# Optimization experiments

Measured on AMD Instinct MI355X. Metric: run time of the kernel, lower is better.

Reference implementation:

```python
import jax, jax.numpy as jnp
import numpy as np

L, B, T, D, H, FF = 4, 8, 1024, 256, 8, 1024
DK = D // H
SCALE = 1.0 / np.sqrt(DK)


def _ln(x, g, b, eps=1e-6):
    m = jnp.mean(x, axis=-1, keepdims=True)
    v = jnp.mean(jnp.square(x - m), axis=-1, keepdims=True)
    return (x - m) * jax.lax.rsqrt(v + eps) * g + b


def _l2norm(x, eps=1e-8):
    n = jnp.sqrt(jnp.sum(jnp.square(x), axis=-1, keepdims=True))
    return x / jnp.maximum(n, eps)


def setup_inputs() -> dict:
    key = jax.random.key(0)
    ks = jax.random.split(key, 8)
    s = 0.02
    inp = {
        'x': jax.random.normal(ks[0], (B, T, D), dtype=jnp.float32),
        'padding_mask': jnp.zeros((B, T), dtype=bool),
        'ln1_g': jnp.ones((L, D), jnp.float32), 'ln1_b': jnp.zeros((L, D), jnp.float32),
        'qn_g': jnp.ones((L, D), jnp.float32), 'qn_b': jnp.zeros((L, D), jnp.float32),
        'Wqkv': jax.random.normal(ks[1], (L, 3 * D, D), jnp.float32) * s,
        'bqkv': jnp.zeros((L, 3 * D), jnp.float32),
        'Wo': jax.random.normal(ks[2], (L, D, D), jnp.float32) * s,
        'bo': jnp.zeros((L, D), jnp.float32),
        'ln2_g': jnp.ones((L, D), jnp.float32), 'ln2_b': jnp.zeros((L, D), jnp.float32),
        'W1': jax.random.normal(ks[3], (L, FF, D), jnp.float32) * s,
        'b1': jnp.zeros((L, FF), jnp.float32),
        'W2': jax.random.normal(ks[4], (L, D, FF), jnp.float32) * s,
        'b2': jnp.zeros((L, D), jnp.float32),
        'alpha': jnp.full((L,), 0.1, jnp.float32),
        'beta': jnp.full((L,), 0.1, jnp.float32),
    }
    return inp


def _block(x, pad_mask, p):
    (g1, bb1, qg, qb, wqkv, bqkv, wo, bo, g2, bb2, w1, b1, w2, b2, a, be) = p
    Bn, Tn, Dn = x.shape
    # --- SemiCausalAttention on norm1(x) ---
    xn = _ln(x, g1, bb1)
    h = _ln(xn, qg, qb)                      # q_norm LayerNorm
    qkv = h @ wqkv.T + bqkv                  # [B,T,3D]
    qkv = qkv.reshape(Bn, Tn, 3, H, DK).transpose(2, 0, 3, 1, 4)  # [3,B,H,T,dk]
    Q, K, V = qkv[0], qkv[1], qkv[2]
    Q = _l2norm(Q)
    K = _l2norm(K)
    scores = jnp.einsum('bhtd,bhsd->bhts', Q, K) * SCALE
    scores = jnp.clip(scores, -10.0, 10.0)
    causal = jnp.triu(jnp.ones((Tn, Tn), dtype=bool), k=1)        # True = future
    scores = jnp.where(causal[None, None], -10000.0, scores)
    scores = jnp.where(pad_mask[:, None, None, :], -10000.0, scores)
    attn = jax.nn.softmax(scores, axis=-1)
    ao = jnp.einsum('bhts,bhsd->bhtd', attn, V)                   # [B,H,T,dk]
    ao = ao.transpose(0, 2, 1, 3).reshape(Bn, Tn, Dn)
    attn_out = (ao @ wo.T + bo) * 0.5
    x = x + jnp.tanh(a) * attn_out
    # --- FFN ---
    f = _ln(x, g2, bb2)
    f = jax.nn.gelu(f @ w1.T + b1, approximate=False)
    f = f @ w2.T + b2
    x = x + jnp.tanh(be) * f
    return jnp.clip(x, -100.0, 100.0)


def reference(x, padding_mask, ln1_g, ln1_b, qn_g, qn_b, Wqkv, bqkv, Wo, bo,
              ln2_g, ln2_b, W1, b1, W2, b2, alpha, beta):
    params = (ln1_g, ln1_b, qn_g, qn_b, Wqkv, bqkv, Wo, bo,
              ln2_g, ln2_b, W1, b1, W2, b2, alpha, beta)

    def step(carry, p):
        return _block(carry, padding_mask, p), None

    out, _ = jax.lax.scan(step, x, params)
    return out
```

## Files before the change

kernel.cpp:

```cpp
#include <hip/hip_runtime.h>
#include <hip/hip_bf16.h>
#include <math.h>

#define BB 8
#define TT 1024
#define DD 256
#define HH 8
#define BT 8192

typedef __attribute__((ext_vector_type(4))) float f32x4;
typedef __attribute__((ext_vector_type(16))) float f32x16;
typedef __attribute__((ext_vector_type(8))) short short8;
typedef __attribute__((ext_vector_type(4))) short short4v;
typedef __attribute__((ext_vector_type(8))) __bf16 bf16x8;

__device__ inline float bf2f(short s) {
  unsigned int u = ((unsigned int)(unsigned short)s) << 16;
  return __builtin_bit_cast(float, u);
}
__device__ inline short f2bf(float f) {
  unsigned int u = __builtin_bit_cast(unsigned int, f);
  unsigned int lsb = (u >> 16) & 1u;
  u += 0x7fffu + lsb;
  return (short)(u >> 16);
}
__device__ inline unsigned int cvtpk(float lo, float hi) {
  unsigned int r;
  asm("v_cvt_pk_bf16_f32 %0, %1, %2" : "=v"(r) : "v"(lo), "v"(hi));
  return r;
}

__device__ inline f32x4 mfma16(short8 a, short8 b, f32x4 c) {
  return __builtin_amdgcn_mfma_f32_16x16x32_bf16(
      __builtin_bit_cast(bf16x8, a), __builtin_bit_cast(bf16x8, b), c, 0, 0, 0);
}
__device__ inline f32x16 mfma32(short8 a, short8 b, f32x16 c) {
  return __builtin_amdgcn_mfma_f32_32x32x16_bf16(
      __builtin_bit_cast(bf16x8, a), __builtin_bit_cast(bf16x8, b), c, 0, 0, 0);
}

__device__ inline void gload_lds16(void* lds, const void* g) {
  __builtin_amdgcn_global_load_lds(
      (const __attribute__((address_space(1))) unsigned int*)g,
      (__attribute__((address_space(3))) unsigned int*)lds, 16, 0, 0);
}

__global__ __launch_bounds__(256) void cvt_all(
    const float4* __restrict__ s0, short4v* __restrict__ d0, int n0,
    const float4* __restrict__ s1, short4v* __restrict__ d1, int n1,
    const float4* __restrict__ s2, short4v* __restrict__ d2, int n2,
    const float4* __restrict__ s3, short4v* __restrict__ d3, int n3)
{
  int i = blockIdx.x * 256 + threadIdx.x;
  const float4* s; short4v* d;
  if (i < n0) { s = s0 + i; d = d0 + i; }
  else if ((i -= n0) < n1) { s = s1 + i; d = d1 + i; }
  else if ((i -= n1) < n2) { s = s2 + i; d = d2 + i; }
  else if ((i -= n2) < n3) { s = s3 + i; d = d3 + i; }
  else return;
  float4 v = *s;
  short4v o;
  o[0] = f2bf(v.x); o[1] = f2bf(v.y); o[2] = f2bf(v.z); o[3] = f2bf(v.w);
  *d = o;
}

__global__ __launch_bounds__(256) void ln_kernel(
    const float* __restrict__ Xin,
    const float* __restrict__ g1, const float* __restrict__ b1,
    const float* __restrict__ g2, const float* __restrict__ b2,
    short* __restrict__ out, int dbl)
{
  const int row = blockIdx.x * 4 + (threadIdx.x >> 6);
  const int lane = threadIdx.x & 63;
  const float4 v = *(const float4*)(Xin + (size_t)row * 256 + lane * 4);
  float y[4] = {v.x, v.y, v.z, v.w};

  float s = y[0] + y[1] + y[2] + y[3];
  #pragma unroll
  for (int m = 32; m >= 1; m >>= 1) s += __shfl_xor(s, m, 64);
  float mean = s * (1.0f / 256.0f);
  float sq = 0.f;
  #pragma unroll
  for (int i = 0; i < 4; ++i) { y[i] -= mean; sq += y[i] * y[i]; }
  #pragma unroll
  for (int m = 32; m >= 1; m >>= 1) sq += __shfl_xor(sq, m, 64);
  float rs = rsqrtf(sq * (1.0f / 256.0f) + 1e-6f);
  #pragma unroll
  for (int i = 0; i < 4; ++i) y[i] = y[i] * rs * g1[lane * 4 + i] + b1[lane * 4 + i];

  if (dbl) {
    float s2 = y[0] + y[1] + y[2] + y[3];
    #pragma unroll
    for (int m = 32; m >= 1; m >>= 1) s2 += __shfl_xor(s2, m, 64);
    float m2 = s2 * (1.0f / 256.0f);
    float sq2 = 0.f;
    #pragma unroll
    for (int i = 0; i < 4; ++i) { y[i] -= m2; sq2 += y[i] * y[i]; }
    #pragma unroll
    for (int m = 32; m >= 1; m >>= 1) sq2 += __shfl_xor(sq2, m, 64);
    float rs2 = rsqrtf(sq2 * (1.0f / 256.0f) + 1e-6f);
    #pragma unroll
    for (int i = 0; i < 4; ++i) y[i] = y[i] * rs2 * g2[lane * 4 + i] + b2[lane * 4 + i];
  }
  #pragma unroll
  for (int i = 0; i < 4; ++i) out[(size_t)row * 256 + lane * 4 + i] = f2bf(y[i]);
}

template<int BN, int EPI>
__global__ __launch_bounds__(256) void gemm_bt(
    const short* __restrict__ A, const short* __restrict__ Bw,
    const float* __restrict__ bias, float* __restrict__ X,
    short* __restrict__ Obf, const float* __restrict__ scale_p,
    int M, int N, int K)
{
  constexpr int MI = (BN == 128) ? 4 : 2;
  __shared__ __align__(16) short A_s[128 * 64];
  __shared__ __align__(16) short B_s[BN * 64];
  const int tid = threadIdx.x;
  const int lane = tid & 63;
  const int w = tid >> 6;
  const int lo4 = lane & 15, hi2 = lane >> 4;
  int wm, wn0;
  if (BN == 128) { wm = (w >> 1) * 64; wn0 = (w & 1) * 64; }
  else           { wm = w * 32;        wn0 = 0; }
  const int bid = blockIdx.x + blockIdx.y * gridDim.x;
  const int nwg = gridDim.x * gridDim.y;
  const int wg = (bid & 7) * (nwg >> 3) + (bid >> 3);
  const int tM = (wg / gridDim.x) * 128, tN = (wg % gridDim.x) * BN;

  f32x4 acc[MI][4];
  #pragma unroll
  for (int i = 0; i < MI; ++i)
    #pragma unroll
    for (int j = 0; j < 4; ++j) acc[i][j] = (f32x4){0.f, 0.f, 0.f, 0.f};

  const int swz = (lo4 & 7) << 3;

  for (int k0 = 0; k0 < K; k0 += 64) {
    #pragma unroll
    for (int ri = 0; ri < 4; ++ri) {
      int o = ri * 2048 + tid * 8;
      int row = o >> 6;
      int col = (o & 63) ^ ((row & 7) << 3);
      gload_lds16(&A_s[ri * 2048 + w * 512], A + (size_t)(tM + row) * K + k0 + col);
    }
    #pragma unroll
    for (int ri = 0; ri < BN / 32; ++ri) {
      int o = ri * 2048 + tid * 8;
      int row = o >> 6;
      int col = (o & 63) ^ ((row & 7) << 3);
      gload_lds16(&B_s[ri * 2048 + w * 512], Bw + (size_t)(tN + row) * K + k0 + col);
    }
    __syncthreads();
    #pragma unroll
    for (int kc = 0; kc < 2; ++kc) {
      short8 af[MI], bfr[4];
      #pragma unroll
      for (int i = 0; i < MI; ++i)
        af[i] = *(const short8*)&A_s[(wm + i * 16 + lo4) * 64 + ((kc * 32 + hi2 * 8) ^ swz)];
      #pragma unroll
      for (int j = 0; j < 4; ++j)
        bfr[j] = *(const short8*)&B_s[(wn0 + j * 16 + lo4) * 64 + ((kc * 32 + hi2 * 8) ^ swz)];
      #pragma unroll
      for (int i = 0; i < MI; ++i)
        #pragma unroll
        for (int j = 0; j < 4; ++j)
          acc[i][j] = mfma16(af[i], bfr[j], acc[i][j]);
    }
    __syncthreads();
  }

  if (EPI == 4) {
    #pragma unroll
    for (int i = 0; i < MI; ++i)
      #pragma unroll
      for (int j = 0; j < 4; ++j)
        #pragma unroll
        for (int r = 0; r < 4; ++r)
          acc[i][j][r] += bias[tN + wn0 + j * 16 + lo4];
    if (tN < 512) {
      const float C2 = 0.25503489702966368f;
      const float sc = (tN < 256) ? C2 : 1.0f;
      #pragma unroll
      for (int i = 0; i < MI; ++i) {
        #pragma unroll
        for (int r = 0; r < 4; ++r) {
          float s01 = acc[i][0][r] * acc[i][0][r] + acc[i][1][r] * acc[i][1][r];
          float s23 = acc[i][2][r] * acc[i][2][r] + acc[i][3][r] * acc[i][3][r];
          #pragma unroll
          for (int m = 1; m <= 8; m <<= 1) {
            s01 += __shfl_xor(s01, m, 64);
            s23 += __shfl_xor(s23, m, 64);
          }
          float n01 = sc / fmaxf(sqrtf(s01), 1e-8f);
          float n23 = sc / fmaxf(sqrtf(s23), 1e-8f);
          acc[i][0][r] *= n01; acc[i][1][r] *= n01;
          acc[i][2][r] *= n23; acc[i][3][r] *= n23;
        }
      }
    }
    #pragma unroll
    for (int i = 0; i < MI; ++i)
      #pragma unroll
      for (int j = 0; j < 4; ++j)
        #pragma unroll
        for (int r = 0; r < 4; ++r) {
          int row = tM + wm + i * 16 + hi2 * 4 + r;
          int col = tN + wn0 + j * 16 + lo4;
          Obf[(size_t)row * N + col] = f2bf(acc[i][j][r]);
        }
    return;
  }

  #pragma unroll
  for (int i = 0; i < MI; ++i) {
    #pragma unroll
    for (int j = 0; j < 4; ++j) {
      #pragma unroll
      for (int r = 0; r < 4; ++r) {
        int row = tM + wm + i * 16 + hi2 * 4 + r;
        int col = tN + wn0 + j * 16 + lo4;
        float v = acc[i][j][r] + bias[col];
        size_t idx = (size_t)row * N + col;
        if (EPI == 2) {
          float gl = 0.5f * v * (1.0f + erff(v * 0.70710678118f));
          Obf[idx] = f2bf(gl);
        } else {
          Obf[idx] = f2bf(v);
        }
      }
    }
  }
}

template<int EPI>
__global__ __launch_bounds__(256) void gemm64(
    const short* __restrict__ A, const short* __restrict__ Bw,
    const float* __restrict__ bias, float* __restrict__ X,
    const float* __restrict__ scale_p, int M, int N, int K)
{
  __shared__ __align__(16) short A_s[64 * 64];
  __shared__ __align__(16) short B_s[64 * 64];
  const int tid = threadIdx.x;
  const int lane = tid & 63;
  const int w = tid >> 6;
  const int lo4 = lane & 15, hi2 = lane >> 4;
  const int wm = (w >> 1) * 32, wn0 = (w & 1) * 32;
  const int bid = blockIdx.x + blockIdx.y * gridDim.x;
  const int nwg = gridDim.x * gridDim.y;
  const int wg = (bid & 7) * (nwg >> 3) + (bid >> 3);
  const int tM = (wg / gridDim.x) * 64, tN = (wg % gridDim.x) * 64;

  f32x4 acc[2][2];
  #pragma unroll
  for (int i = 0; i < 2; ++i)
    #pragma unroll
    for (int j = 0; j < 2; ++j) acc[i][j] = (f32x4){0.f, 0.f, 0.f, 0.f};

  const int swz = (lo4 & 7) << 3;

  for (int k0 = 0; k0 < K; k0 += 64) {
    #pragma unroll
    for (int ri = 0; ri < 2; ++ri) {
      int o = ri * 2048 + tid * 8;
      int row = o >> 6;
      int col = (o & 63) ^ ((row & 7) << 3);
      gload_lds16(&A_s[ri * 2048 + w * 512], A + (size_t)(tM + row) * K + k0 + col);
      gload_lds16(&B_s[ri * 2048 + w * 512], Bw + (size_t)(tN + row) * K + k0 + col);
    }
    __syncthreads();
    #pragma unroll
    for (int kc = 0; kc < 2; ++kc) {
      short8 af[2], bfr[2];
      #pragma unroll
      for (int i = 0; i < 2; ++i)
        af[i] = *(const short8*)&A_s[(wm + i * 16 + lo4) * 64 + ((kc * 32 + hi2 * 8) ^ swz)];
      #pragma unroll
      for (int j = 0; j < 2; ++j)
        bfr[j] = *(const short8*)&B_s[(wn0 + j * 16 + lo4) * 64 + ((kc * 32 + hi2 * 8) ^ swz)];
      #pragma unroll
      for (int i = 0; i < 2; ++i)
        #pragma unroll
        for (int j = 0; j < 2; ++j)
          acc[i][j] = mfma16(af[i], bfr[j], acc[i][j]);
    }
    __syncthreads();
  }

  float ts = tanhf(scale_p[0]);

  #pragma unroll
  for (int i = 0; i < 2; ++i) {
    #pragma unroll
    for (int j = 0; j < 2; ++j) {
      #pragma unroll
      for (int r = 0; r < 4; ++r) {
        int row = tM + wm + i * 16 + hi2 * 4 + r;
        int col = tN + wn0 + j * 16 + lo4;
        float v = acc[i][j][r] + bias[col];
        size_t idx = (size_t)row * N + col;
        if (EPI == 1) {
          X[idx] += ts * (v * 0.5f);
        } else {
          float o = X[idx] + ts * v;
          o = fminf(100.f, fmaxf(-100.f, o));
          X[idx] = o;
        }
      }
    }
  }
}

#define KG_BODY_G(KG, PKO, MASKED)                                                 \
  {                                                                                \
    const short* kp = Kbase + (size_t)(t * 64 + (KG) * 32 + lo5) * 768;            \
    short8 kf0 = *(const short8*)(kp + hi1 * 8);                                   \
    short8 kf1 = *(const short8*)(kp + 16 + hi1 * 8);                              \
    f32x16 z = (f32x16)0.0f;                                                       \
    z = mfma32(kf0, qb[0], z);                                                     \
    z = mfma32(kf1, qb[1], z);                                                     \
    float pr[16];                                                                  \
    _Pragma("unroll")                                                              \
    for (int r = 0; r < 16; ++r) {                                                 \
      float sv = __builtin_amdgcn_fmed3f(z[r], -14.4269504f, 14.4269504f);         \
      float pe;                                                                    \
      asm("v_exp_f32 %0, %1" : "=v"(pe) : "v"(sv));                                \
      const int keyrel = (r & 3) + 8 * (r >> 2) + 4 * hi1;                         \
      if (MASKED) pe = (keyrel > lo5) ? 0.f : pe;                                  \
      if (pm) pe = ((pm >> ((KG) * 32 + keyrel)) & 1ull) ? 0.f : pe;               \
      pr[r] = pe;                                                                  \
      rsum += pe;                                                                  \
    }                                                                              \
    _Pragma("unroll")                                                              \
    for (int i = 0; i < 8; ++i) PKO[i] = cvtpk(pr[2 * i], pr[2 * i + 1]);          \
  }

#define PV_CHUNK_G(K2, PKO)                                                        \
  {                                                                                \
    const int half_ = (K2) & 1;                                                    \
    unsigned int keep0 = hi1 ? PKO[4 * half_ + 2] : PKO[4 * half_ + 0];            \
    unsigned int keep1 = hi1 ? PKO[4 * half_ + 3] : PKO[4 * half_ + 1];            \
    unsigned int send0 = hi1 ? PKO[4 * half_ + 0] : PKO[4 * half_ + 2];            \
    unsigned int send1 = hi1 ? PKO[4 * half_ + 1] : PKO[4 * half_ + 3];            \
    unsigned int r0 = (unsigned int)__shfl_xor((int)send0, 32, 64);                \
    unsigned int r1 = (unsigned int)__shfl_xor((int)send1, 32, 64);                \
    union { unsigned int u[4]; short8 s; } fa;                                     \
    fa.u[0] = hi1 ? r0 : keep0;                                                    \
    fa.u[1] = hi1 ? r1 : keep1;                                                    \
    fa.u[2] = hi1 ? keep0 : r0;                                                    \
    fa.u[3] = hi1 ? keep1 : r1;                                                    \
    short8 vb;                                                                     \
    _Pragma("unroll")                                                              \
    for (int jj = 0; jj < 8; ++jj)                                                 \
      vb[jj] = Vbase[(size_t)(t * 64 + (K2) * 16 + hi1 * 8 + jj) * 768 + lo5];     \
    if ((K2) & 1) oaccB = mfma32(fa.s, vb, oaccB);                                 \
    else          oaccA = mfma32(fa.s, vb, oaccA);                                 \
  }

__global__ __launch_bounds__(256, 2) void attn_kernel(
    const short* __restrict__ qkv, const unsigned char* __restrict__ pad,
    short* __restrict__ ao)
{
  __shared__ float Red[2][17][64];
  const int tid = threadIdx.x, lane = tid & 63, w = tid >> 6;
  const int lo5 = lane & 31, hi1 = lane >> 5;
  const int bid = blockIdx.x;
  const int b = bid & 7;
  const int h = (bid >> 3) & 7;
  const int bj = bid >> 6;
  const int p = w >> 1;
  const int half = w & 1;
  const int j = p ? (31 - bj) : bj;
  const size_t rowbase = (size_t)b * TT;
  const int qrow = j * 32 + lo5;
  const int ntile = (j >> 1) + 1;

  const short* Kbase = qkv + rowbase * 768 + 256 + h * 32;
  const short* Vbase = qkv + rowbase * 768 + 512 + h * 32;

  const ulonglong2 pv = *(const ulonglong2*)(pad + rowbase + lane * 16);
  const unsigned long long anyp = __ballot((pv.x | pv.y) != 0ull);

  short8 qb[2];
  #pragma unroll
  for (int c2 = 0; c2 < 2; ++c2)
    qb[c2] = *(const short8*)(qkv + (rowbase + qrow) * 768 + h * 32 + c2 * 16 + hi1 * 8);

  f32x16 oaccA = (f32x16)0.0f;
  f32x16 oaccB = (f32x16)0.0f;
  float rsum = 0.f;

  for (int t = half; t < ntile; t += 2) {
    unsigned long long pm = 0;
    if ((anyp >> (4 * t)) & 0xFull)
      pm = __ballot(pad[rowbase + t * 64 + lane] != 0);
    unsigned int pk0[8], pk1[8];
    if (t + 1 < ntile) {
      KG_BODY_G(0, pk0, false)
      PV_CHUNK_G(0, pk0)
      PV_CHUNK_G(1, pk0)
      KG_BODY_G(1, pk1, false)
      PV_CHUNK_G(2, pk1)
      PV_CHUNK_G(3, pk1)
    } else if (j & 1) {
      KG_BODY_G(0, pk0, false)
      PV_CHUNK_G(0, pk0)
      PV_CHUNK_G(1, pk0)
      KG_BODY_G(1, pk1, true)
      PV_CHUNK_G(2, pk1)
      PV_CHUNK_G(3, pk1)
    } else {
      KG_BODY_G(0, pk0, true)
      PV_CHUNK_G(0, pk0)
      PV_CHUNK_G(1, pk0)
    }
  }

  if (half) {
    #pragma unroll
    for (int r = 0; r < 16; ++r) Red[p][r][lane] = oaccA[r] + oaccB[r];
    Red[p][16][lane] = rsum;
  }
  __syncthreads();
  if (!half) {
    #pragma unroll
    for (int r = 0; r < 16; ++r) oaccA[r] += oaccB[r] + Red[p][r][lane];
    rsum += Red[p][16][lane];
    rsum += __shfl_xor(rsum, 32, 64);
    float rinv = 1.0f / fmaxf(rsum, 1e-30f);
    #pragma unroll
    for (int r = 0; r < 16; ++r) {
      int ql = (r & 3) + 8 * (r >> 2) + 4 * hi1;
      float riv = __shfl(rinv, ql, 64);
      int qg = j * 32 + ql;
      ao[(rowbase + qg) * 256 + h * 32 + lo5] = f2bf(oaccA[r] * riv);
    }
  }
}

extern "C" void kernel_launch(void* const* d_in, const int* in_sizes, int n_in,
                              void* d_out, int out_size, void* d_ws, size_t ws_size,
                              hipStream_t stream) {
  const float* x_in  = (const float*)d_in[0];
  const unsigned char* pad = (const unsigned char*)d_in[1];
  const float* ln1_g = (const float*)d_in[2];
  const float* ln1_b = (const float*)d_in[3];
  const float* qn_g  = (const float*)d_in[4];
  const float* qn_b  = (const float*)d_in[5];
  const float* Wqkv  = (const float*)d_in[6];
  const float* bqkv  = (const float*)d_in[7];
  const float* Wo    = (const float*)d_in[8];
  const float* bo    = (const float*)d_in[9];
  const float* ln2_g = (const float*)d_in[10];
  const float* ln2_b = (const float*)d_in[11];
  const float* W1    = (const float*)d_in[12];
  const float* b1    = (const float*)d_in[13];
  const float* W2    = (const float*)d_in[14];
  const float* b2    = (const float*)d_in[15];
  const float* alpha = (const float*)d_in[16];
  const float* beta  = (const float*)d_in[17];

  char* ws = (char*)d_ws;
  size_t off = 0;
  short* wqkv_bf = (short*)(ws + off); off += (size_t)4 * 768 * 256 * 2;
  short* wo_bf   = (short*)(ws + off); off += (size_t)4 * 256 * 256 * 2;
  short* w1_bf   = (short*)(ws + off); off += (size_t)4 * 1024 * 256 * 2;
  short* w2_bf   = (short*)(ws + off); off += (size_t)4 * 256 * 1024 * 2;
  short* h_bf    = (short*)(ws + off); off += (size_t)BT * 256 * 2;
  short* qkv_bf  = (short*)(ws + off); off += (size_t)BT * 768 * 2;
  short* ao_bf   = (short*)(ws + off); off += (size_t)BT * 256 * 2;
  short* g_bf    = (short*)(ws + off); off += (size_t)BT * 1024 * 2;

  float* X = (float*)d_out;

  hipMemcpyAsync(d_out, x_in, (size_t)BT * DD * 4, hipMemcpyDeviceToDevice, stream);
  cvt_all<<<3072, 256, 0, stream>>>(
      (const float4*)Wqkv, (short4v*)wqkv_bf, 4 * 768 * 256 / 4,
      (const float4*)Wo,   (short4v*)wo_bf,   4 * 256 * 256 / 4,
      (const float4*)W1,   (short4v*)w1_bf,   4 * 1024 * 256 / 4,
      (const float4*)W2,   (short4v*)w2_bf,   4 * 256 * 1024 / 4);

  for (int l = 0; l < 4; ++l) {
    ln_kernel<<<2048, 256, 0, stream>>>(X, ln1_g + l * 256, ln1_b + l * 256,
                                        qn_g + l * 256, qn_b + l * 256, h_bf, 1);
    gemm_bt<128, 4><<<dim3(6, 64), 256, 0, stream>>>(h_bf, wqkv_bf + (size_t)l * 768 * 256,
                                                     bqkv + l * 768, nullptr, qkv_bf, nullptr,
                                                     8192, 768, 256);
    attn_kernel<<<1024, 256, 0, stream>>>(qkv_bf, pad, ao_bf);
    gemm64<1><<<dim3(4, 128), 256, 0, stream>>>(ao_bf, wo_bf + (size_t)l * 256 * 256,
                                                bo + l * 256, X, alpha + l,
                                                8192, 256, 256);
    ln_kernel<<<2048, 256, 0, stream>>>(X, ln2_g + l * 256, ln2_b + l * 256,
                                        nullptr, nullptr, h_bf, 0);
    gemm_bt<128, 2><<<dim3(8, 64), 256, 0, stream>>>(h_bf, w1_bf + (size_t)l * 1024 * 256,
                                                     b1 + l * 1024, nullptr, g_bf, nullptr,
                                                     8192, 1024, 256);
    gemm64<3><<<dim3(4, 128), 256, 0, stream>>>(g_bf, w2_bf + (size_t)l * 256 * 1024,
                                                b2 + l * 256, X, beta + l,
                                                8192, 256, 1024);
  }
}
```

Baseline: 388.8 us.

## Fuse LayerNorms into full-row output GEMM epilogues and restructure attention tile loads

The Wo and W2 projection GEMMs now use 32x256 tiles that cover whole rows, so the residual update, the following LayerNorm (double LN for the next layer's attention input) and the bf16 conversion happen in the epilogue. This drops the separate ln_kernel launches and the extra read of X they needed. The attention inner loop is rewritten as a templated function that issues all K and V loads for a tile before the exp/MFMA work, to overlap load latency. The trade-offs are a grid of only 256 blocks with each block loading all 256 weight rows per k-step, and LayerNorm variance now computed as E[x^2]-mu^2.

Result: faster. 380.5 us (-2.2%).

```diff
diff --git a/kernel.cpp b/kernel.cpp
--- a/kernel.cpp
+++ b/kernel.cpp
@@ -68,7 +68,7 @@
     const float* __restrict__ Xin,
     const float* __restrict__ g1, const float* __restrict__ b1,
     const float* __restrict__ g2, const float* __restrict__ b2,
-    short* __restrict__ out, int dbl)
+    short* __restrict__ out)
 {
   const int row = blockIdx.x * 4 + (threadIdx.x >> 6);
   const int lane = threadIdx.x & 63;
@@ -88,20 +88,19 @@
   #pragma unroll
   for (int i = 0; i < 4; ++i) y[i] = y[i] * rs * g1[lane * 4 + i] + b1[lane * 4 + i];
 
-  if (dbl) {
-    float s2 = y[0] + y[1] + y[2] + y[3];
-    #pragma unroll
-    for (int m = 32; m >= 1; m >>= 1) s2 += __shfl_xor(s2, m, 64);
-    float m2 = s2 * (1.0f / 256.0f);
-    float sq2 = 0.f;
-    #pragma unroll
-    for (int i = 0; i < 4; ++i) { y[i] -= m2; sq2 += y[i] * y[i]; }
-    #pragma unroll
-    for (int m = 32; m >= 1; m >>= 1) sq2 += __shfl_xor(sq2, m, 64);
-    float rs2 = rsqrtf(sq2 * (1.0f / 256.0f) + 1e-6f);
-    #pragma unroll
-    for (int i = 0; i < 4; ++i) y[i] = y[i] * rs2 * g2[lane * 4 + i] + b2[lane * 4 + i];
-  }
+  float s2 = y[0] + y[1] + y[2] + y[3];
+  #pragma unroll
+  for (int m = 32; m >= 1; m >>= 1) s2 += __shfl_xor(s2, m, 64);
+  float m2 = s2 * (1.0f / 256.0f);
+  float sq2 = 0.f;
+  #pragma unroll
+  for (int i = 0; i < 4; ++i) { y[i] -= m2; sq2 += y[i] * y[i]; }
+  #pragma unroll
+  for (int m = 32; m >= 1; m >>= 1) sq2 += __shfl_xor(sq2, m, 64);
+  float rs2 = rsqrtf(sq2 * (1.0f / 256.0f) + 1e-6f);
+  #pragma unroll
+  for (int i = 0; i < 4; ++i) y[i] = y[i] * rs2 * g2[lane * 4 + i] + b2[lane * 4 + i];
+
   #pragma unroll
   for (int i = 0; i < 4; ++i) out[(size_t)row * 256 + lane * 4 + i] = f2bf(y[i]);
 }
@@ -233,129 +232,251 @@
   }
 }
 
-template<int EPI>
-__global__ __launch_bounds__(256) void gemm64(
+template<int MODE>
+__global__ __launch_bounds__(256) void gemm_ln(
     const short* __restrict__ A, const short* __restrict__ Bw,
     const float* __restrict__ bias, float* __restrict__ X,
-    const float* __restrict__ scale_p, int M, int N, int K)
+    short* __restrict__ Obf, const float* __restrict__ scale_p,
+    const float* __restrict__ gA, const float* __restrict__ bA,
+    const float* __restrict__ gB, const float* __restrict__ bB,
+    int K, int doLN)
 {
-  __shared__ __align__(16) short A_s[64 * 64];
-  __shared__ __align__(16) short B_s[64 * 64];
+  __shared__ __align__(16) short A_s[32 * 64];
+  __shared__ __align__(16) short B_s[256 * 64];
+  __shared__ float Red[2][32][4][2];
   const int tid = threadIdx.x;
   const int lane = tid & 63;
   const int w = tid >> 6;
   const int lo4 = lane & 15, hi2 = lane >> 4;
-  const int wm = (w >> 1) * 32, wn0 = (w & 1) * 32;
-  const int bid = blockIdx.x + blockIdx.y * gridDim.x;
-  const int nwg = gridDim.x * gridDim.y;
-  const int wg = (bid & 7) * (nwg >> 3) + (bid >> 3);
-  const int tM = (wg / gridDim.x) * 64, tN = (wg % gridDim.x) * 64;
-
-  f32x4 acc[2][2];
+  const int tM = blockIdx.x * 32;
+  const int swz = (lo4 & 7) << 3;
+
+  f32x4 acc[2][4];
   #pragma unroll
   for (int i = 0; i < 2; ++i)
     #pragma unroll
-    for (int j = 0; j < 2; ++j) acc[i][j] = (f32x4){0.f, 0.f, 0.f, 0.f};
-
-  const int swz = (lo4 & 7) << 3;
+    for (int j = 0; j < 4; ++j) acc[i][j] = (f32x4){0.f, 0.f, 0.f, 0.f};
 
   for (int k0 = 0; k0 < K; k0 += 64) {
-    #pragma unroll
-    for (int ri = 0; ri < 2; ++ri) {
+    {
+      int o = tid * 8;
+      int row = o >> 6;
+      int col = (o & 63) ^ ((row & 7) << 3);
+      gload_lds16(&A_s[w * 512], A + (size_t)(tM + row) * K + k0 + col);
+    }
+    #pragma unroll
+    for (int ri = 0; ri < 8; ++ri) {
       int o = ri * 2048 + tid * 8;
       int row = o >> 6;
       int col = (o & 63) ^ ((row & 7) << 3);
-      gload_lds16(&A_s[ri * 2048 + w * 512], A + (size_t)(tM + row) * K + k0 + col);
-      gload_lds16(&B_s[ri * 2048 + w * 512], Bw + (size_t)(tN + row) * K + k0 + col);
+      gload_lds16(&B_s[ri * 2048 + w * 512], Bw + (size_t)row * K + k0 + col);
     }
     __syncthreads();
     #pragma unroll
     for (int kc = 0; kc < 2; ++kc) {
-      short8 af[2], bfr[2];
+      short8 af[2], bfr[4];
       #pragma unroll
       for (int i = 0; i < 2; ++i)
-        af[i] = *(const short8*)&A_s[(wm + i * 16 + lo4) * 64 + ((kc * 32 + hi2 * 8) ^ swz)];
-      #pragma unroll
-      for (int j = 0; j < 2; ++j)
-        bfr[j] = *(const short8*)&B_s[(wn0 + j * 16 + lo4) * 64 + ((kc * 32 + hi2 * 8) ^ swz)];
+        af[i] = *(const short8*)&A_s[(i * 16 + lo4) * 64 + ((kc * 32 + hi2 * 8) ^ swz)];
+      #pragma unroll
+      for (int j = 0; j < 4; ++j)
+        bfr[j] = *(const short8*)&B_s[(w * 64 + j * 16 + lo4) * 64 + ((kc * 32 + hi2 * 8) ^ swz)];
       #pragma unroll
       for (int i = 0; i < 2; ++i)
         #pragma unroll
-        for (int j = 0; j < 2; ++j)
+        for (int j = 0; j < 4; ++j)
           acc[i][j] = mfma16(af[i], bfr[j], acc[i][j]);
     }
     __syncthreads();
   }
 
-  float ts = tanhf(scale_p[0]);
-
-  #pragma unroll
-  for (int i = 0; i < 2; ++i) {
-    #pragma unroll
-    for (int j = 0; j < 2; ++j) {
+  const float ts = tanhf(scale_p[0]);
+  float xv[2][4][4];
+  #pragma unroll
+  for (int i = 0; i < 2; ++i)
+    #pragma unroll
+    for (int j = 0; j < 4; ++j)
       #pragma unroll
       for (int r = 0; r < 4; ++r) {
-        int row = tM + wm + i * 16 + hi2 * 4 + r;
-        int col = tN + wn0 + j * 16 + lo4;
+        int row = i * 16 + hi2 * 4 + r;
+        int col = w * 64 + j * 16 + lo4;
         float v = acc[i][j][r] + bias[col];
-        size_t idx = (size_t)row * N + col;
-        if (EPI == 1) {
-          X[idx] += ts * (v * 0.5f);
+        size_t idx = (size_t)(tM + row) * 256 + col;
+        float xn;
+        if (MODE == 0) {
+          xn = X[idx] + ts * 0.5f * v;
         } else {
-          float o = X[idx] + ts * v;
-          o = fminf(100.f, fmaxf(-100.f, o));
-          X[idx] = o;
+          xn = X[idx] + ts * v;
+          xn = fminf(100.f, fmaxf(-100.f, xn));
+        }
+        X[idx] = xn;
+        xv[i][j][r] = xn;
+      }
+
+  if (!doLN) return;
+
+  #pragma unroll
+  for (int i = 0; i < 2; ++i)
+    #pragma unroll
+    for (int r = 0; r < 4; ++r) {
+      float s = xv[i][0][r] + xv[i][1][r] + xv[i][2][r] + xv[i][3][r];
+      float q = xv[i][0][r] * xv[i][0][r] + xv[i][1][r] * xv[i][1][r]
+              + xv[i][2][r] * xv[i][2][r] + xv[i][3][r] * xv[i][3][r];
+      #pragma unroll
+      for (int m = 1; m <= 8; m <<= 1) { s += __shfl_xor(s, m, 64); q += __shfl_xor(q, m, 64); }
+      if (lo4 == 0) { Red[0][i * 16 + hi2 * 4 + r][w][0] = s; Red[0][i * 16 + hi2 * 4 + r][w][1] = q; }
+    }
+  __syncthreads();
+  #pragma unroll
+  for (int i = 0; i < 2; ++i)
+    #pragma unroll
+    for (int r = 0; r < 4; ++r) {
+      int row = i * 16 + hi2 * 4 + r;
+      float s = Red[0][row][0][0] + Red[0][row][1][0] + Red[0][row][2][0] + Red[0][row][3][0];
+      float q = Red[0][row][0][1] + Red[0][row][1][1] + Red[0][row][2][1] + Red[0][row][3][1];
+      float mu = s * (1.0f / 256.0f);
+      float var = q * (1.0f / 256.0f) - mu * mu;
+      float rs = rsqrtf(var + 1e-6f);
+      #pragma unroll
+      for (int j = 0; j < 4; ++j) {
+        int col = w * 64 + j * 16 + lo4;
+        xv[i][j][r] = (xv[i][j][r] - mu) * rs * gA[col] + bA[col];
+      }
+    }
+
+  if (MODE == 1) {
+    #pragma unroll
+    for (int i = 0; i < 2; ++i)
+      #pragma unroll
+      for (int r = 0; r < 4; ++r) {
+        float s = xv[i][0][r] + xv[i][1][r] + xv[i][2][r] + xv[i][3][r];
+        float q = xv[i][0][r] * xv[i][0][r] + xv[i][1][r] * xv[i][1][r]
+                + xv[i][2][r] * xv[i][2][r] + xv[i][3][r] * xv[i][3][r];
+        #pragma unroll
+        for (int m = 1; m <= 8; m <<= 1) { s += __shfl_xor(s, m, 64); q += __shfl_xor(q, m, 64); }
+        if (lo4 == 0) { Red[1][i * 16 + hi2 * 4 + r][w][0] = s; Red[1][i * 16 + hi2 * 4 + r][w][1] = q; }
+      }
+    __syncthreads();
+    #pragma unroll
+    for (int i = 0; i < 2; ++i)
+      #pragma unroll
+      for (int r = 0; r < 4; ++r) {
+        int row = i * 16 + hi2 * 4 + r;
+        float s = Red[1][row][0][0] + Red[1][row][1][0] + Red[1][row][2][0] + Red[1][row][3][0];
+        float q = Red[1][row][0][1] + Red[1][row][1][1] + Red[1][row][2][1] + Red[1][row][3][1];
+        float mu = s * (1.0f / 256.0f);
+        float var = q * (1.0f / 256.0f) - mu * mu;
+        float rs = rsqrtf(var + 1e-6f);
+        #pragma unroll
+        for (int j = 0; j < 4; ++j) {
+          int col = w * 64 + j * 16 + lo4;
+          xv[i][j][r] = (xv[i][j][r] - mu) * rs * gB[col] + bB[col];
         }
       }
-    }
-  }
-}
-
-#define KG_BODY_G(KG, PKO, MASKED)                                                 \
-  {                                                                                \
-    const short* kp = Kbase + (size_t)(t * 64 + (KG) * 32 + lo5) * 768;            \
-    short8 kf0 = *(const short8*)(kp + hi1 * 8);                                   \
-    short8 kf1 = *(const short8*)(kp + 16 + hi1 * 8);                              \
-    f32x16 z = (f32x16)0.0f;                                                       \
-    z = mfma32(kf0, qb[0], z);                                                     \
-    z = mfma32(kf1, qb[1], z);                                                     \
-    float pr[16];                                                                  \
-    _Pragma("unroll")                                                              \
-    for (int r = 0; r < 16; ++r) {                                                 \
-      float sv = __builtin_amdgcn_fmed3f(z[r], -14.4269504f, 14.4269504f);         \
-      float pe;                                                                    \
-      asm("v_exp_f32 %0, %1" : "=v"(pe) : "v"(sv));                                \
-      const int keyrel = (r & 3) + 8 * (r >> 2) + 4 * hi1;                         \
-      if (MASKED) pe = (keyrel > lo5) ? 0.f : pe;                                  \
-      if (pm) pe = ((pm >> ((KG) * 32 + keyrel)) & 1ull) ? 0.f : pe;               \
-      pr[r] = pe;                                                                  \
-      rsum += pe;                                                                  \
-    }                                                                              \
-    _Pragma("unroll")                                                              \
-    for (int i = 0; i < 8; ++i) PKO[i] = cvtpk(pr[2 * i], pr[2 * i + 1]);          \
-  }
-
-#define PV_CHUNK_G(K2, PKO)                                                        \
-  {                                                                                \
-    const int half_ = (K2) & 1;                                                    \
-    unsigned int keep0 = hi1 ? PKO[4 * half_ + 2] : PKO[4 * half_ + 0];            \
-    unsigned int keep1 = hi1 ? PKO[4 * half_ + 3] : PKO[4 * half_ + 1];            \
-    unsigned int send0 = hi1 ? PKO[4 * half_ + 0] : PKO[4 * half_ + 2];            \
-    unsigned int send1 = hi1 ? PKO[4 * half_ + 1] : PKO[4 * half_ + 3];            \
-    unsigned int r0 = (unsigned int)__shfl_xor((int)send0, 32, 64);                \
-    unsigned int r1 = (unsigned int)__shfl_xor((int)send1, 32, 64);                \
-    union { unsigned int u[4]; short8 s; } fa;                                     \
-    fa.u[0] = hi1 ? r0 : keep0;                                                    \
-    fa.u[1] = hi1 ? r1 : keep1;                                                    \
-    fa.u[2] = hi1 ? keep0 : r0;                                                    \
-    fa.u[3] = hi1 ? keep1 : r1;                                                    \
-    short8 vb;                                                                     \
-    _Pragma("unroll")                                                              \
-    for (int jj = 0; jj < 8; ++jj)                                                 \
-      vb[jj] = Vbase[(size_t)(t * 64 + (K2) * 16 + hi1 * 8 + jj) * 768 + lo5];     \
-    if ((K2) & 1) oaccB = mfma32(fa.s, vb, oaccB);                                 \
-    else          oaccA = mfma32(fa.s, vb, oaccA);                                 \
-  }
+  }
+
+  #pragma unroll
+  for (int i = 0; i < 2; ++i)
+    #pragma unroll
+    for (int j = 0; j < 4; ++j)
+      #pragma unroll
+      for (int r = 0; r < 4; ++r) {
+        int row = i * 16 + hi2 * 4 + r;
+        int col = w * 64 + j * 16 + lo4;
+        Obf[(size_t)(tM + row) * 256 + col] = f2bf(xv[i][j][r]);
+      }
+}
+
+__device__ __forceinline__ void pv_acc(const unsigned int* PKO, int half_,
+                                       short8 vb, int hi1, f32x16& acc) {
+  unsigned int keep0 = hi1 ? PKO[4 * half_ + 2] : PKO[4 * half_ + 0];
+  unsigned int keep1 = hi1 ? PKO[4 * half_ + 3] : PKO[4 * half_ + 1];
+  unsigned int send0 = hi1 ? PKO[4 * half_ + 0] : PKO[4 * half_ + 2];
+  unsigned int send1 = hi1 ? PKO[4 * half_ + 1] : PKO[4 * half_ + 3];
+  unsigned int r0 = (unsigned int)__shfl_xor((int)send0, 32, 64);
+  unsigned int r1 = (unsigned int)__shfl_xor((int)send1, 32, 64);
+  union { unsigned int u[4]; short8 s; } fa;
+  fa.u[0] = hi1 ? r0 : keep0;
+  fa.u[1] = hi1 ? r1 : keep1;
+  fa.u[2] = hi1 ? keep0 : r0;
+  fa.u[3] = hi1 ? keep1 : r1;
+  acc = mfma32(fa.s, vb, acc);
+}
+
+template<bool KG1, bool M0, bool M1>
+__device__ __forceinline__ void attn_tile(
+    int t, const short* __restrict__ Kbase, const short* __restrict__ Vbase,
+    const short8* qb, unsigned int pm0, unsigned int pm1, int lo5, int hi1,
+    f32x16& oaccA, f32x16& oaccB, float& rsum)
+{
+  const short* kp0 = Kbase + (size_t)(t * 64 + lo5) * 768;
+  short8 k00 = *(const short8*)(kp0 + hi1 * 8);
+  short8 k01 = *(const short8*)(kp0 + 16 + hi1 * 8);
+  short8 k10, k11;
+  if (KG1) {
+    const short* kp1 = Kbase + (size_t)(t * 64 + 32 + lo5) * 768;
+    k10 = *(const short8*)(kp1 + hi1 * 8);
+    k11 = *(const short8*)(kp1 + 16 + hi1 * 8);
+  }
+  short8 vb0, vb1, vb2, vb3;
+  #pragma unroll
+  for (int jj = 0; jj < 8; ++jj) {
+    vb0[jj] = Vbase[(size_t)(t * 64 + 0 + hi1 * 8 + jj) * 768 + lo5];
+    vb1[jj] = Vbase[(size_t)(t * 64 + 16 + hi1 * 8 + jj) * 768 + lo5];
+  }
+  if (KG1) {
+    #pragma unroll
+    for (int jj = 0; jj < 8; ++jj) {
+      vb2[jj] = Vbase[(size_t)(t * 64 + 32 + hi1 * 8 + jj) * 768 + lo5];
+      vb3[jj] = Vbase[(size_t)(t * 64 + 48 + hi1 * 8 + jj) * 768 + lo5];
+    }
+  }
+  unsigned int pk0[8], pk1[8];
+  {
+    f32x16 z = (f32x16)0.0f;
+    z = mfma32(k00, qb[0], z);
+    z = mfma32(k01, qb[1], z);
+    float pr[16];
+    #pragma unroll
+    for (int r = 0; r < 16; ++r) {
+      float sv = __builtin_amdgcn_fmed3f(z[r], -14.4269504f, 14.4269504f);
+      float pe;
+      asm("v_exp_f32 %0, %1" : "=v"(pe) : "v"(sv));
+      const int keyrel = (r & 3) + 8 * (r >> 2) + 4 * hi1;
+      if (M0) pe = (keyrel > lo5) ? 0.f : pe;
+      if (pm0) pe = ((pm0 >> keyrel) & 1u) ? 0.f : pe;
+      pr[r] = pe;
+      rsum += pe;
+    }
+    #pragma unroll
+    for (int i = 0; i < 8; ++i) pk0[i] = cvtpk(pr[2 * i], pr[2 * i + 1]);
+  }
+  if (KG1) {
+    f32x16 z = (f32x16)0.0f;
+    z = mfma32(k10, qb[0], z);
+    z = mfma32(k11, qb[1], z);
+    float pr[16];
+    #pragma unroll
+    for (int r = 0; r < 16; ++r) {
+      float sv = __builtin_amdgcn_fmed3f(z[r], -14.4269504f, 14.4269504f);
+      float pe;
+      asm("v_exp_f32 %0, %1" : "=v"(pe) : "v"(sv));
+      const int keyrel = (r & 3) + 8 * (r >> 2) + 4 * hi1;
+      if (M1) pe = (keyrel > lo5) ? 0.f : pe;
+      if (pm1) pe = ((pm1 >> keyrel) & 1u) ? 0.f : pe;
+      pr[r] = pe;
+      rsum += pe;
+    }
+    #pragma unroll
+    for (int i = 0; i < 8; ++i) pk1[i] = cvtpk(pr[2 * i], pr[2 * i + 1]);
+  }
+  pv_acc(pk0, 0, vb0, hi1, oaccA);
+  pv_acc(pk0, 1, vb1, hi1, oaccB);
+  if (KG1) {
+    pv_acc(pk1, 0, vb2, hi1, oaccA);
+    pv_acc(pk1, 1, vb3, hi1, oaccB);
+  }
+}
 
 __global__ __launch_bounds__(256, 2) void attn_kernel(
     const short* __restrict__ qkv, const unsigned char* __restrict__ pad,
@@ -394,26 +515,13 @@
     unsigned long long pm = 0;
     if ((anyp >> (4 * t)) & 0xFull)
       pm = __ballot(pad[rowbase + t * 64 + lane] != 0);
-    unsigned int pk0[8], pk1[8];
-    if (t + 1 < ntile) {
-      KG_BODY_G(0, pk0, false)
-      PV_CHUNK_G(0, pk0)
-      PV_CHUNK_G(1, pk0)
-      KG_BODY_G(1, pk1, false)
-      PV_CHUNK_G(2, pk1)
-      PV_CHUNK_G(3, pk1)
-    } else if (j & 1) {
-      KG_BODY_G(0, pk0, false)
-      PV_CHUNK_G(0, pk0)
-      PV_CHUNK_G(1, pk0)
-      KG_BODY_G(1, pk1, true)
-      PV_CHUNK_G(2, pk1)
-      PV_CHUNK_G(3, pk1)
-    } else {
-      KG_BODY_G(0, pk0, true)
-      PV_CHUNK_G(0, pk0)
-      PV_CHUNK_G(1, pk0)
-    }
+    unsigned int pm0 = (unsigned int)pm, pm1 = (unsigned int)(pm >> 32);
+    if (t + 1 < ntile)
+      attn_tile<true, false, false>(t, Kbase, Vbase, qb, pm0, pm1, lo5, hi1, oaccA, oaccB, rsum);
+    else if (j & 1)
+      attn_tile<true, false, true>(t, Kbase, Vbase, qb, pm0, pm1, lo5, hi1, oaccA, oaccB, rsum);
+    else
+      attn_tile<false, true, false>(t, Kbase, Vbase, qb, pm0, pm1, lo5, hi1, oaccA, oaccB, rsum);
   }
 
   if (half) {
@@ -480,23 +588,25 @@
       (const float4*)W1,   (short4v*)w1_bf,   4 * 1024 * 256 / 4,
       (const float4*)W2,   (short4v*)w2_bf,   4 * 256 * 1024 / 4);
 
+  ln_kernel<<<2048, 256, 0, stream>>>(X, ln1_g, ln1_b, qn_g, qn_b, h_bf);
+
   for (int l = 0; l < 4; ++l) {
-    ln_kernel<<<2048, 256, 0, stream>>>(X, ln1_g + l * 256, ln1_b + l * 256,
-                                        qn_g + l * 256, qn_b + l * 256, h_bf, 1);
     gemm_bt<128, 4><<<dim3(6, 64), 256, 0, stream>>>(h_bf, wqkv_bf + (size_t)l * 768 * 256,
                                                      bqkv + l * 768, nullptr, qkv_bf, nullptr,
                                                      8192, 768, 256);
     attn_kernel<<<1024, 256, 0, stream>>>(qkv_bf, pad, ao_bf);
-    gemm64<1><<<dim3(4, 128), 256, 0, stream>>>(ao_bf, wo_bf + (size_t)l * 256 * 256,
-                                                bo + l * 256, X, alpha + l,
-                                                8192, 256, 256);
-    ln_kernel<<<2048, 256, 0, stream>>>(X, ln2_g + l * 256, ln2_b + l * 256,
-                                        nullptr, nullptr, h_bf, 0);
+    gemm_ln<0><<<256, 256, 0, stream>>>(ao_bf, wo_bf + (size_t)l * 256 * 256,
+                                        bo + l * 256, X, h_bf, alpha + l,
+                                        ln2_g + l * 256, ln2_b + l * 256,
+                                        nullptr, nullptr, 256, 1);
     gemm_bt<128, 2><<<dim3(8, 64), 256, 0, stream>>>(h_bf, w1_bf + (size_t)l * 1024 * 256,
                                                      b1 + l * 1024, nullptr, g_bf, nullptr,
                                                      8192, 1024, 256);
-    gemm64<3><<<dim3(4, 128), 256, 0, stream>>>(g_bf, w2_bf + (size_t)l * 256 * 1024,
-                                                b2 + l * 256, X, beta + l,
-                                                8192, 256, 1024);
-  }
-}
+    const int nl = (l < 3) ? (l + 1) : 0;
+    gemm_ln<1><<<256, 256, 0, stream>>>(g_bf, w2_bf + (size_t)l * 256 * 1024,
+                                        b2 + l * 256, X, h_bf, beta + l,
+                                        ln1_g + nl * 256, ln1_b + nl * 256,
+                                        qn_g + nl * 256, qn_b + nl * 256,
+                                        1024, (l < 3) ? 1 : 0);
+  }
+}
```
